# Kernel tuning notes

Measured on AMD Instinct MI355X. Metric: run time of the kernel, lower is better.

Reference implementation:

```python
import jax, jax.numpy as jnp
import numpy as np

T, N, L_DIM, P_DIM = 8192, 4096, 64, 32
IN_DIM = 3 * L_DIM  # library = [identity, square, sin]
MIN_TEMP, ALPHA, REP_COEF = 0.01, 0.999, 0.1


def build_library(X):
    # (T, L) -> (T, 3L): concatenated library features
    return jnp.concatenate([X, X * X, jnp.sin(X)], axis=1)


def setup_inputs() -> dict:
    key = jax.random.key(0)
    k = jax.random.split(key, 8)
    u = jax.random.uniform(k[6], (P_DIM, IN_DIM), minval=1e-7, maxval=1.0)
    return {
        "X_tilde_t_batch": jax.random.normal(k[0], (T, L_DIM), jnp.float32),
        "X_train_t_batch": jax.random.normal(k[1], (T, N), jnp.float32),
        "Y_train_t_batch": jax.random.normal(k[2], (T, N), jnp.float32),
        "temp": jnp.ones((1,), jnp.float32),
        "phi_bar_t": jax.random.normal(k[3], (P_DIM, L_DIM), jnp.float32) * 0.01,
        # spectral radius ~0.9 so the 8192-step linear recurrence stays bounded
        "A_tilde": jax.random.normal(k[4], (L_DIM, L_DIM), jnp.float32) * (0.9 / np.sqrt(L_DIM)),
        "U_l": jax.random.normal(k[5], (N, L_DIM), jnp.float32) / np.sqrt(N),
        "logits": jax.random.normal(k[7], (P_DIM, IN_DIM), jnp.float32),
        "gumbel_g": -jnp.log(-jnp.log(u)),  # Gumbel(0,1) noise, precomputed
    }


def reference(X_tilde_t_batch, X_train_t_batch, Y_train_t_batch, temp,
              phi_bar_t, A_tilde, U_l, logits, gumbel_g):
    # --- GumbelSelector (train=True) ---
    X_mod = build_library(X_tilde_t_batch)                           # (T, 3L)
    new_temp = jnp.maximum(MIN_TEMP, temp[0] * ALPHA)
    soft = jax.nn.softmax((logits + gumbel_g) / new_temp, axis=-1)   # (P, 3L)
    X_sel = X_mod @ soft.T                                           # (T, P) -- computed but unused downstream, as in source
    selected_idx = jnp.argmax(logits, axis=-1)                       # (P,)
    probs = jax.nn.softmax(logits, axis=-1)
    l0_pen = REP_COEF * jnp.sum(jnp.max(probs, axis=-1))             # computed, unused (as in source)

    # --- reconstruction_error: sequential linear state-space recurrence ---
    x0 = X_train_t_batch[0]                                          # (N,)  first column of X_train_batch
    xh0 = U_l.T @ x0                                                 # (L,)  projected initial state
    phi_bar = phi_bar_t.T                                            # (L, P)

    def step(xh, _):
        mod_sel = jnp.take(xh, selected_idx, mode='clip')            # (P,) irregular gather (clip matches jit take)
        xh = A_tilde @ xh + phi_bar @ mod_sel                        # tiny matvecs
        return xh, xh

    _, xh_seq = jax.lax.scan(step, xh0, None, length=T)              # (T, L)
    X_rec = xh_seq @ U_l.T                                           # (T, N) == (U_r @ xh_seq.T).T with U_r = U_l
    # Frobenius norm is transpose-invariant, so compute in (T, N) layout
    err = jnp.linalg.norm(Y_train_t_batch - X_rec) / jnp.linalg.norm(Y_train_t_batch)
    return (X_rec, err, new_temp, selected_idx)
```

## Files before the change

kernel.cpp:

```cpp
#include <hip/hip_runtime.h>
#include <math.h>

#define T_DIM 8192
#define N_DIM 4096
#define L 64
#define P 32
#define IN_DIM 192
#define S_CHUNK 16
#define N_CHUNK (T_DIM / S_CHUNK)
#define LDST 68

using f32x4   = __attribute__((ext_vector_type(4))) float;
using bf16x8  = __attribute__((ext_vector_type(8))) short;
using ushort8 = __attribute__((ext_vector_type(8))) unsigned short;

__device__ __forceinline__ unsigned short f2bf(float x) {
  unsigned u = __float_as_uint(x);
  u += 0x7fffu + ((u >> 16) & 1u);
  return (unsigned short)(u >> 16);
}
__device__ __forceinline__ float bf2f(unsigned short h) {
  return __uint_as_float(((unsigned)h) << 16);
}

__global__ __launch_bounds__(64) void k_xh0_part(const float* __restrict__ U,
                                                 const float* __restrict__ Xtr,
                                                 float* __restrict__ part,
                                                 double* __restrict__ acc) {
  int b = blockIdx.x;
  int l = threadIdx.x;
  if (b == 0 && l < 2) acc[l] = 0.0;
  int n0 = b * 64;
  float s = 0.f;
  #pragma unroll 8
  for (int i = 0; i < 64; ++i) {
    float x = Xtr[n0 + i];
    s += U[(size_t)(n0 + i) * L + l] * x;
  }
  part[b * 64 + l] = s;
}

__global__ __launch_bounds__(256) void k_usplit(const float* __restrict__ U,
                                                unsigned short* __restrict__ uh,
                                                unsigned short* __restrict__ ul) {
  int i = blockIdx.x * 256 + threadIdx.x;
  float4 x = ((const float4*)U)[i];
  ushort4 h, lo;
  h.x = f2bf(x.x); lo.x = f2bf(x.x - bf2f(h.x));
  h.y = f2bf(x.y); lo.y = f2bf(x.y - bf2f(h.y));
  h.z = f2bf(x.z); lo.z = f2bf(x.z - bf2f(h.z));
  h.w = f2bf(x.w); lo.w = f2bf(x.w - bf2f(h.w));
  ((ushort4*)uh)[i] = h;
  ((ushort4*)ul)[i] = lo;
}

__global__ __launch_bounds__(256, 1) void k_prep(const float* __restrict__ A_tilde,
                                                 const float* __restrict__ phi_bar_t,
                                                 const float* __restrict__ logits,
                                                 const float* __restrict__ temp,
                                                 const float* __restrict__ part,
                                                 float* __restrict__ Wm,
                                                 float* __restrict__ xh0,
                                                 float* __restrict__ out_tail) {
  __shared__ float buf[2][64 * LDST];
  __shared__ float sphi[P * L];
  __shared__ float spart[4 * 64];
  __shared__ int   sel_s[P];
  int tid = threadIdx.x;

  #pragma unroll
  for (int i = 0; i < 4; ++i) {
    int f = tid + 256 * i;
    int r = f >> 4, q = f & 15;
    float4 v = ((const float4*)A_tilde)[f];
    *(float4*)(buf[0] + r * LDST + q * 4) = v;
  }
  #pragma unroll
  for (int i = 0; i < 2; ++i) {
    int f = tid + 256 * i;
    ((float4*)sphi)[f] = ((const float4*)phi_bar_t)[f];
  }
  {
    int l = tid & 63, q = tid >> 6;
    float s = 0.f;
    #pragma unroll
    for (int i = 0; i < 16; ++i)
      s += part[(q * 16 + i) * 64 + l];
    spart[q * 64 + l] = s;
  }
  {
    int p = tid >> 3, d = tid & 7;
    const float* row = logits + p * IN_DIM;
    float best = -1e30f; int bk = 0;
    #pragma unroll
    for (int j = 0; j < 6; ++j) {
      int kb = (j * 8 + d) * 4;
      float4 v = *(const float4*)(row + kb);
      if (v.x > best) { best = v.x; bk = kb; }
      if (v.y > best) { best = v.y; bk = kb + 1; }
      if (v.z > best) { best = v.z; bk = kb + 2; }
      if (v.w > best) { best = v.w; bk = kb + 3; }
    }
    #pragma unroll
    for (int off = 4; off > 0; off >>= 1) {
      float vo = __shfl_down(best, off, 8);
      int   ko = __shfl_down(bk,   off, 8);
      if (vo > best || (vo == best && ko < bk)) { best = vo; bk = ko; }
    }
    if (d == 0) {
      sel_s[p] = bk;
      out_tail[2 + p] = (float)bk;
    }
  }
  if (tid == 255) out_tail[1] = fmaxf(0.01f, temp[0] * 0.999f);
  __syncthreads();

  if (tid < L) {
    #pragma unroll 4
    for (int p = 0; p < P; ++p) {
      int kk = sel_s[p]; if (kk > L - 1) kk = L - 1;
      buf[0][tid * LDST + kk] += sphi[p * L + tid];
    }
  } else if (tid < 128) {
    int l = tid - 64;
    xh0[l] = spart[l] + spart[64 + l] + spart[128 + l] + spart[192 + l];
  }
  __syncthreads();

  #pragma unroll
  for (int i = 0; i < 4; ++i) {
    int f = tid + 256 * i;
    int r = f >> 4, q = f & 15;
    *(float4*)(Wm + r * 64 + q * 4) = *(const float4*)(buf[0] + r * LDST + q * 4);
  }

  int r0 = (tid >> 4) << 2;
  int c0 = (tid & 15) << 2;
  int cur = 0;
  for (int j = 1; j <= 12; ++j) {
    const float* S = buf[cur];
    float* D = buf[cur ^ 1];
    float acc[4][4];
    #pragma unroll
    for (int i = 0; i < 4; ++i)
      #pragma unroll
      for (int c = 0; c < 4; ++c) acc[i][c] = 0.f;

    #pragma unroll
    for (int kb = 0; kb < 64; kb += 16) {
      float a[4][16];
      #pragma unroll
      for (int i = 0; i < 4; ++i)
        #pragma unroll
        for (int q = 0; q < 4; ++q) {
          float4 t4 = *(const float4*)(S + (r0 + i) * LDST + kb + q * 4);
          a[i][q * 4 + 0] = t4.x; a[i][q * 4 + 1] = t4.y;
          a[i][q * 4 + 2] = t4.z; a[i][q * 4 + 3] = t4.w;
        }
      #pragma unroll
      for (int kk = 0; kk < 16; ++kk) {
        float4 b4 = *(const float4*)(S + (kb + kk) * LDST + c0);
        #pragma unroll
        for (int i = 0; i < 4; ++i) {
          acc[i][0] += a[i][kk] * b4.x;
          acc[i][1] += a[i][kk] * b4.y;
          acc[i][2] += a[i][kk] * b4.z;
          acc[i][3] += a[i][kk] * b4.w;
        }
      }
    }
    #pragma unroll
    for (int i = 0; i < 4; ++i) {
      float4 o = {acc[i][0], acc[i][1], acc[i][2], acc[i][3]};
      *(float4*)(D + (r0 + i) * LDST + c0) = o;
      *(float4*)(Wm + j * 4096 + (r0 + i) * 64 + c0) = o;
    }
    __syncthreads();
    cur ^= 1;
  }
}

__global__ __launch_bounds__(64) void k_states(const float* __restrict__ Wm,
                                               const float* __restrict__ xh0,
                                               unsigned short* __restrict__ xhi,
                                               unsigned short* __restrict__ xlo) {
  int c = blockIdx.x;
  int l = threadIdx.x;
  float v = xh0[l];
  int e = c << 4;
  for (int j = 4; j <= 12; ++j) {
    if ((e >> j) & 1) {
      const float* W = Wm + j * 4096;
      float n0 = 0.f, n1 = 0.f, n2 = 0.f, n3 = 0.f;
      #pragma unroll
      for (int k = 0; k < 64; k += 4) {
        n0 += W[l * 64 + k]     * __shfl(v, k, 64);
        n1 += W[l * 64 + k + 1] * __shfl(v, k + 1, 64);
        n2 += W[l * 64 + k + 2] * __shfl(v, k + 2, 64);
        n3 += W[l * 64 + k + 3] * __shfl(v, k + 3, 64);
      }
      v = (n0 + n1) + (n2 + n3);
    }
  }
  float m[64];
  #pragma unroll
  for (int k = 0; k < 64; ++k) m[k] = Wm[l * 64 + k];
  int t0 = c * S_CHUNK;
  for (int i = 0; i < S_CHUNK; ++i) {
    float n0 = 0.f, n1 = 0.f, n2 = 0.f, n3 = 0.f;
    #pragma unroll
    for (int k = 0; k < 64; k += 4) {
      n0 += m[k]     * __shfl(v, k, 64);
      n1 += m[k + 1] * __shfl(v, k + 1, 64);
      n2 += m[k + 2] * __shfl(v, k + 2, 64);
      n3 += m[k + 3] * __shfl(v, k + 3, 64);
    }
    v = (n0 + n1) + (n2 + n3);
    unsigned short h = f2bf(v);
    unsigned short lo = f2bf(v - bf2f(h));
    size_t base = (size_t)(t0 + i) * L + l;
    xhi[base] = h; xlo[base] = lo;
  }
}

__global__ __launch_bounds__(256, 2) void k_xrec(const unsigned short* __restrict__ xhi,
                                                 const unsigned short* __restrict__ xlo,
                                                 const unsigned short* __restrict__ uh,
                                                 const unsigned short* __restrict__ ul,
                                                 const float* __restrict__ Y,
                                                 float* __restrict__ Xrec,
                                                 double* __restrict__ acc_g) {
  __shared__ __align__(16) unsigned short Xs[128 * 128];
  __shared__ __align__(16) unsigned short Us[128 * 128];
  __shared__ float red[512];

  int tid = threadIdx.x;
  int nt = blockIdx.x & 31, tt = blockIdx.x >> 5;
  int n0 = nt * 128, t0 = tt * 128;

  #pragma unroll
  for (int i = 0; i < 8; ++i) {
    int c = tid + 256 * i;
    int t = c >> 4, p = c & 15;
    const ushort8* src = (p < 8)
      ? (const ushort8*)(xhi + (size_t)(t0 + t) * L + p * 8)
      : (const ushort8*)(xlo + (size_t)(t0 + t) * L + (p - 8) * 8);
    *(ushort8*)((char*)Xs + t * 256 + ((p * 16) ^ ((t & 7) << 4))) = *src;
  }
  #pragma unroll
  for (int i = 0; i < 8; ++i) {
    int c = tid + 256 * i;
    int nn = c >> 4, p = c & 15;
    const ushort8* src = (p < 8)
      ? (const ushort8*)(uh + (size_t)(n0 + nn) * L + p * 8)
      : (const ushort8*)(ul + (size_t)(n0 + nn) * L + (p - 8) * 8);
    *(ushort8*)((char*)Us + nn * 256 + ((p * 16) ^ ((nn & 7) << 4))) = *src;
  }
  __syncthreads();

  int l = tid & 63, wid = tid >> 6;
  int wr = wid >> 1, wc = wid & 1;
  int lr = l & 15, lg = l >> 4;

  f32x4 acc[4][4];
  #pragma unroll
  for (int m = 0; m < 4; ++m)
    #pragma unroll
    for (int nf = 0; nf < 4; ++nf) acc[m][nf] = (f32x4){0.f, 0.f, 0.f, 0.f};

  const int KA[6] = {0, 32, 64, 96, 0, 32};
  const int KB[6] = {0, 32, 0, 32, 64, 96};
  #pragma unroll
  for (int s = 0; s < 6; ++s) {
    bf16x8 af[4], bfr[4];
    #pragma unroll
    for (int m = 0; m < 4; ++m) {
      int t_loc = wr * 64 + m * 16 + lr;
      int kk = KA[s] + lg * 8;
      af[m] = *(const bf16x8*)((const char*)Xs + t_loc * 256 + ((kk * 2) ^ ((t_loc & 7) << 4)));
    }
    #pragma unroll
    for (int nf = 0; nf < 4; ++nf) {
      int n_loc = wc * 64 + nf * 16 + lr;
      int kk = KB[s] + lg * 8;
      bfr[nf] = *(const bf16x8*)((const char*)Us + n_loc * 256 + ((kk * 2) ^ ((n_loc & 7) << 4)));
    }
    #pragma unroll
    for (int m = 0; m < 4; ++m)
      #pragma unroll
      for (int nf = 0; nf < 4; ++nf)
        acc[m][nf] = __builtin_amdgcn_mfma_f32_16x16x32_bf16(af[m], bfr[nf], acc[m][nf], 0, 0, 0);
  }

  float sd = 0.f, sy = 0.f;
  #pragma unroll
  for (int m = 0; m < 4; ++m) {
    #pragma unroll
    for (int nf = 0; nf < 4; ++nf) {
      #pragma unroll
      for (int r = 0; r < 4; ++r) {
        int t = t0 + wr * 64 + m * 16 + lg * 4 + r;
        int n = n0 + wc * 64 + nf * 16 + lr;
        size_t idx = (size_t)t * N_DIM + n;
        float x = acc[m][nf][r];
        float y = Y[idx];
        float d = y - x;
        sd += d * d; sy += y * y;
        Xrec[idx] = x;
      }
    }
  }

  red[tid] = sd; red[256 + tid] = sy;
  __syncthreads();
  for (int s2 = 128; s2 > 0; s2 >>= 1) {
    if (tid < s2) { red[tid] += red[tid + s2]; red[256 + tid] += red[256 + tid + s2]; }
    __syncthreads();
  }
  if (tid == 0) {
    atomicAdd(acc_g,     (double)red[0]);
    atomicAdd(acc_g + 1, (double)red[256]);
  }
}

__global__ void k_err(const double* __restrict__ acc, float* __restrict__ out_tail) {
  out_tail[0] = (float)sqrt(acc[0] / acc[1]);
}

extern "C" void kernel_launch(void* const* d_in, const int* in_sizes, int n_in,
                              void* d_out, int out_size, void* d_ws, size_t ws_size,
                              hipStream_t stream) {
  const float* X_train = (const float*)d_in[1];
  const float* Y       = (const float*)d_in[2];
  const float* temp    = (const float*)d_in[3];
  const float* phi     = (const float*)d_in[4];
  const float* A_tilde = (const float*)d_in[5];
  const float* U       = (const float*)d_in[6];
  const float* logits  = (const float*)d_in[7];
  float* out = (float*)d_out;
  float* out_tail = out + (size_t)T_DIM * N_DIM;

  char* w = (char*)d_ws;
  double* acc          = (double*)w;
  float* Wm            = (float*)(w + 64);
  float* xh0           = (float*)(w + 213056);
  float* part          = (float*)(w + 213312);
  unsigned short* uh   = (unsigned short*)(w + 262144);
  unsigned short* ul   = (unsigned short*)(w + 786432);
  unsigned short* xhi  = (unsigned short*)(w + 1310720);
  unsigned short* xlo  = (unsigned short*)(w + 2359296);

  k_xh0_part<<<64, 64, 0, stream>>>(U, X_train, part, acc);
  k_usplit<<<(N_DIM * L / 4) / 256, 256, 0, stream>>>(U, uh, ul);
  k_prep<<<1, 256, 0, stream>>>(A_tilde, phi, logits, temp, part, Wm, xh0, out_tail);
  k_states<<<N_CHUNK, 64, 0, stream>>>(Wm, xh0, xhi, xlo);
  k_xrec<<<2048, 256, 0, stream>>>(xhi, xlo, uh, ul, Y, out, acc);
  k_err<<<1, 1, 0, stream>>>(acc, out_tail);
}
```

Baseline: 127.8 us.

## Stage MFMA output through LDS for coalesced stores, fuse init and error kernels

The xrec epilogue now writes the accumulator tiles into a swizzled LDS staging buffer, with MFMA operands swapped to transpose the fragment layout. It then reads Y and writes Xrec as contiguous float4 rows instead of scattered scalar accesses. The xh0 partial sum and U bf16 split kernels are merged into one launch, and the final error kernel is replaced by a last-block-done counter inside xrec. This removes two launches and improves global memory coalescing, at the cost of extra LDS traffic and barriers.

```diff
diff --git a/kernel.cpp b/kernel.cpp
--- a/kernel.cpp
+++ b/kernel.cpp
@@ -23,35 +23,42 @@
   return __uint_as_float(((unsigned)h) << 16);
 }
 
-__global__ __launch_bounds__(64) void k_xh0_part(const float* __restrict__ U,
-                                                 const float* __restrict__ Xtr,
-                                                 float* __restrict__ part,
-                                                 double* __restrict__ acc) {
-  int b = blockIdx.x;
-  int l = threadIdx.x;
-  if (b == 0 && l < 2) acc[l] = 0.0;
-  int n0 = b * 64;
-  float s = 0.f;
-  #pragma unroll 8
-  for (int i = 0; i < 64; ++i) {
-    float x = Xtr[n0 + i];
-    s += U[(size_t)(n0 + i) * L + l] * x;
-  }
-  part[b * 64 + l] = s;
-}
-
-__global__ __launch_bounds__(256) void k_usplit(const float* __restrict__ U,
-                                                unsigned short* __restrict__ uh,
-                                                unsigned short* __restrict__ ul) {
-  int i = blockIdx.x * 256 + threadIdx.x;
-  float4 x = ((const float4*)U)[i];
-  ushort4 h, lo;
-  h.x = f2bf(x.x); lo.x = f2bf(x.x - bf2f(h.x));
-  h.y = f2bf(x.y); lo.y = f2bf(x.y - bf2f(h.y));
-  h.z = f2bf(x.z); lo.z = f2bf(x.z - bf2f(h.z));
-  h.w = f2bf(x.w); lo.w = f2bf(x.w - bf2f(h.w));
-  ((ushort4*)uh)[i] = h;
-  ((ushort4*)ul)[i] = lo;
+#define MFMA(A, B, C) __builtin_amdgcn_mfma_f32_16x16x32_bf16(A, B, C, 0, 0, 0)
+
+__global__ __launch_bounds__(256) void k_init(const float* __restrict__ U,
+                                              const float* __restrict__ Xtr,
+                                              float* __restrict__ part,
+                                              double* __restrict__ acc,
+                                              int* __restrict__ cnt,
+                                              unsigned short* __restrict__ uh,
+                                              unsigned short* __restrict__ ul) {
+  int blk = blockIdx.x, tid = threadIdx.x;
+  if (blk < 16) {
+    if (blk == 0) {
+      if (tid < 2) acc[tid] = 0.0;
+      if (tid == 2) *cnt = 0;
+    }
+    int b = blk * 4 + (tid >> 6);
+    int l = tid & 63;
+    int n0 = b * 64;
+    float s = 0.f;
+    #pragma unroll 8
+    for (int i = 0; i < 64; ++i) {
+      float x = Xtr[n0 + i];
+      s += U[(size_t)(n0 + i) * L + l] * x;
+    }
+    part[b * 64 + l] = s;
+  } else {
+    int i = (blk - 16) * 256 + tid;
+    float4 x = ((const float4*)U)[i];
+    ushort4 h, lo;
+    h.x = f2bf(x.x); lo.x = f2bf(x.x - bf2f(h.x));
+    h.y = f2bf(x.y); lo.y = f2bf(x.y - bf2f(h.y));
+    h.z = f2bf(x.z); lo.z = f2bf(x.z - bf2f(h.z));
+    h.w = f2bf(x.w); lo.w = f2bf(x.w - bf2f(h.w));
+    ((ushort4*)uh)[i] = h;
+    ((ushort4*)ul)[i] = lo;
+  }
 }
 
 __global__ __launch_bounds__(256, 1) void k_prep(const float* __restrict__ A_tilde,
@@ -229,10 +236,14 @@
                                                  const unsigned short* __restrict__ ul,
                                                  const float* __restrict__ Y,
                                                  float* __restrict__ Xrec,
-                                                 double* __restrict__ acc_g) {
-  __shared__ __align__(16) unsigned short Xs[128 * 128];
-  __shared__ __align__(16) unsigned short Us[128 * 128];
+                                                 double* __restrict__ acc_g,
+                                                 int* __restrict__ cnt,
+                                                 float* __restrict__ out_tail) {
+  __shared__ __align__(16) unsigned char smem[65536];
   __shared__ float red[512];
+  unsigned short* Xs = (unsigned short*)smem;
+  unsigned short* Us = (unsigned short*)(smem + 32768);
+  float* stage = (float*)smem;
 
   int tid = threadIdx.x;
   int nt = blockIdx.x & 31, tt = blockIdx.x >> 5;
@@ -289,26 +300,38 @@
     for (int m = 0; m < 4; ++m)
       #pragma unroll
       for (int nf = 0; nf < 4; ++nf)
-        acc[m][nf] = __builtin_amdgcn_mfma_f32_16x16x32_bf16(af[m], bfr[nf], acc[m][nf], 0, 0, 0);
-  }
+        acc[m][nf] = MFMA(bfr[nf], af[m], acc[m][nf]);
+  }
+  __syncthreads();
+
+  #pragma unroll
+  for (int m = 0; m < 4; ++m) {
+    int t_loc = wr * 64 + m * 16 + lr;
+    #pragma unroll
+    for (int nf = 0; nf < 4; ++nf) {
+      int nq = wc * 16 + nf * 4 + lg;
+      int physq = nq ^ (t_loc & 31);
+      *(f32x4*)(stage + t_loc * 128 + physq * 4) = acc[m][nf];
+    }
+  }
+  __syncthreads();
 
   float sd = 0.f, sy = 0.f;
   #pragma unroll
-  for (int m = 0; m < 4; ++m) {
-    #pragma unroll
-    for (int nf = 0; nf < 4; ++nf) {
-      #pragma unroll
-      for (int r = 0; r < 4; ++r) {
-        int t = t0 + wr * 64 + m * 16 + lg * 4 + r;
-        int n = n0 + wc * 64 + nf * 16 + lr;
-        size_t idx = (size_t)t * N_DIM + n;
-        float x = acc[m][nf][r];
-        float y = Y[idx];
-        float d = y - x;
-        sd += d * d; sy += y * y;
-        Xrec[idx] = x;
-      }
-    }
+  for (int p = 0; p < 16; ++p) {
+    int flat = p * 1024 + tid * 4;
+    int row = flat >> 7;
+    int nq2 = (flat >> 2) & 31;
+    int physq = nq2 ^ (row & 31);
+    f32x4 x = *(const f32x4*)(stage + row * 128 + physq * 4);
+    size_t gidx = (size_t)(t0 + row) * N_DIM + n0 + nq2 * 4;
+    float4 y = *(const float4*)(Y + gidx);
+    float d;
+    d = y.x - x[0]; sd += d * d; sy += y.x * y.x;
+    d = y.y - x[1]; sd += d * d; sy += y.y * y.y;
+    d = y.z - x[2]; sd += d * d; sy += y.z * y.z;
+    d = y.w - x[3]; sd += d * d; sy += y.w * y.w;
+    *(f32x4*)(Xrec + gidx) = x;
   }
 
   red[tid] = sd; red[256 + tid] = sy;
@@ -320,11 +343,14 @@
   if (tid == 0) {
     atomicAdd(acc_g,     (double)red[0]);
     atomicAdd(acc_g + 1, (double)red[256]);
-  }
-}
-
-__global__ void k_err(const double* __restrict__ acc, float* __restrict__ out_tail) {
-  out_tail[0] = (float)sqrt(acc[0] / acc[1]);
+    __threadfence();
+    int done = atomicAdd(cnt, 1);
+    if (done == 2047) {
+      double s0 = atomicAdd(acc_g, 0.0);
+      double s1 = atomicAdd(acc_g + 1, 0.0);
+      out_tail[0] = (float)sqrt(s0 / s1);
+    }
+  }
 }
 
 extern "C" void kernel_launch(void* const* d_in, const int* in_sizes, int n_in,
@@ -342,6 +368,7 @@
 
   char* w = (char*)d_ws;
   double* acc          = (double*)w;
+  int* cnt             = (int*)(w + 32);
   float* Wm            = (float*)(w + 64);
   float* xh0           = (float*)(w + 213056);
   float* part          = (float*)(w + 213312);
@@ -350,10 +377,8 @@
   unsigned short* xhi  = (unsigned short*)(w + 1310720);
   unsigned short* xlo  = (unsigned short*)(w + 2359296);
 
-  k_xh0_part<<<64, 64, 0, stream>>>(U, X_train, part, acc);
-  k_usplit<<<(N_DIM * L / 4) / 256, 256, 0, stream>>>(U, uh, ul);
+  k_init<<<80, 256, 0, stream>>>(U, X_train, part, acc, cnt, uh, ul);
   k_prep<<<1, 256, 0, stream>>>(A_tilde, phi, logits, temp, part, Wm, xh0, out_tail);
   k_states<<<N_CHUNK, 64, 0, stream>>>(Wm, xh0, xhi, xlo);
-  k_xrec<<<2048, 256, 0, stream>>>(xhi, xlo, uh, ul, Y, out, acc);
-  k_err<<<1, 1, 0, stream>>>(acc, out_tail);
-}
+  k_xrec<<<2048, 256, 0, stream>>>(xhi, xlo, uh, ul, Y, out, acc, cnt, out_tail);
+}
```

After: 203.0 us. 1.59x slower.
